# Kernel optimization log

Measured on AMD Instinct MI355X. Metric: run time of the kernel, lower is better.

The kernel has to match this reference:

```python
import jax, jax.numpy as jnp
import numpy as np

B, T, S, D, H, FF = 4, 1024, 1024, 1024, 16, 4096
DH = D // H
NEG = -1e9
EPS = 1e-5


def setup_inputs() -> dict:
    key = jax.random.key(0)
    ks = jax.random.split(key, 20)
    p = 0.02  # param init scale
    inp = {
        "x": jax.random.normal(ks[0], (B, T, D), jnp.float32),
        "encoder_output": jax.random.normal(ks[1], (B, S, D), jnp.float32),
        "src_mask": jnp.ones((B, 1, 1, S), jnp.bool_),
        "tgt_mask": jnp.tril(jnp.ones((1, 1, T, T), jnp.bool_)),  # causal
        # self-attention params
        "d_Wq": jax.random.normal(ks[2], (D, D)) * p, "d_bq": jnp.zeros((D,)),
        "d_Wk": jax.random.normal(ks[3], (D, D)) * p, "d_bk": jnp.zeros((D,)),
        "d_Wv": jax.random.normal(ks[4], (D, D)) * p, "d_bv": jnp.zeros((D,)),
        "d_Wo": jax.random.normal(ks[5], (D, D)) * p, "d_bo": jnp.zeros((D,)),
        # cross-attention params
        "e_Wq": jax.random.normal(ks[6], (D, D)) * p, "e_bq": jnp.zeros((D,)),
        "e_Wk": jax.random.normal(ks[7], (D, D)) * p, "e_bk": jnp.zeros((D,)),
        "e_Wv": jax.random.normal(ks[8], (D, D)) * p, "e_bv": jnp.zeros((D,)),
        "e_Wo": jax.random.normal(ks[9], (D, D)) * p, "e_bo": jnp.zeros((D,)),
        # FFN params
        "ff_W1": jax.random.normal(ks[10], (D, FF)) * p, "ff_b1": jnp.zeros((FF,)),
        "ff_W2": jax.random.normal(ks[11], (FF, D)) * p, "ff_b2": jnp.zeros((D,)),
        # layernorm params
        "ln1_g": jnp.ones((D,)), "ln1_b": jnp.zeros((D,)),
        "ln2_g": jnp.ones((D,)), "ln2_b": jnp.zeros((D,)),
        "ln3_g": jnp.ones((D,)), "ln3_b": jnp.zeros((D,)),
    }
    return inp


def _mha(xq, xkv, Wq, bq, Wk, bk, Wv, bv, Wo, bo, mask):
    b, tq = xq.shape[0], xq.shape[1]
    q = (xq @ Wq + bq).reshape(b, tq, H, DH).transpose(0, 2, 1, 3)
    k = (xkv @ Wk + bk).reshape(b, -1, H, DH).transpose(0, 2, 1, 3)
    v = (xkv @ Wv + bv).reshape(b, -1, H, DH).transpose(0, 2, 1, 3)
    scores = jnp.einsum("bhqd,bhkd->bhqk", q, k) / np.float32(np.sqrt(DH))
    scores = jnp.where(mask, scores, NEG)
    attn = jax.nn.softmax(scores, axis=-1)
    out = jnp.einsum("bhqk,bhkd->bhqd", attn, v)
    out = out.transpose(0, 2, 1, 3).reshape(b, tq, D)
    return out @ Wo + bo


def _ln(x, g, b):
    m = jnp.mean(x, axis=-1, keepdims=True)
    v = jnp.var(x, axis=-1, keepdims=True)
    return (x - m) / jnp.sqrt(v + EPS) * g + b


def reference(x, encoder_output, src_mask, tgt_mask,
              d_Wq, d_bq, d_Wk, d_bk, d_Wv, d_bv, d_Wo, d_bo,
              e_Wq, e_bq, e_Wk, e_bk, e_Wv, e_bv, e_Wo, e_bo,
              ff_W1, ff_b1, ff_W2, ff_b2,
              ln1_g, ln1_b, ln2_g, ln2_b, ln3_g, ln3_b):
    # masked self-attention + residual + LN (dropout is identity in eval)
    d = _mha(x, x, d_Wq, d_bq, d_Wk, d_bk, d_Wv, d_bv, d_Wo, d_bo, tgt_mask)
    d = _ln(d + x, ln1_g, ln1_b)
    # cross-attention over encoder output + residual + LN
    f = _mha(d, encoder_output, e_Wq, e_bq, e_Wk, e_bk, e_Wv, e_bv, e_Wo, e_bo, src_mask)
    f = _ln(f + d, ln2_g, ln2_b)
    # FFN + residual + LN
    g = jax.nn.relu(f @ ff_W1 + ff_b1) @ ff_W2 + ff_b2
    g = _ln(g + f, ln3_g, ln3_b)
    return g
```

## Files before the change

### kernel.cpp

```cpp
#include <hip/hip_runtime.h>

static constexpr int Bc = 4, Tc = 1024, Sc = 1024, Dc = 1024, Hc = 16, DHc = 64, FFc = 4096;

typedef __attribute__((ext_vector_type(8))) short short8;
typedef __attribute__((ext_vector_type(4))) short short4v;
typedef __attribute__((ext_vector_type(4))) float f32x4;

struct P8 { unsigned short* o[8]; };

__device__ __forceinline__ unsigned short f2bf(float f) {
    unsigned int u = __float_as_uint(f);
    unsigned int r = u + 0x7fffu + ((u >> 16) & 1u);
    return (unsigned short)(r >> 16);
}
__device__ __forceinline__ float bf2f(unsigned short u) {
    return __uint_as_float(((unsigned int)u) << 16);
}
__device__ __forceinline__ float fexp2(float x) {
    float r; asm("v_exp_f32 %0, %1" : "=v"(r) : "v"(x)); return r;
}
__device__ __forceinline__ unsigned int cvtpk(float a, float b) {
    unsigned int r;
    asm("v_cvt_pk_bf16_f32 %0, %1, %2" : "=v"(r) : "v"(a), "v"(b));
    return r;
}

__device__ __forceinline__ void gload_lds16(const void* g, void* l) {
    __builtin_amdgcn_global_load_lds((const __attribute__((address_space(1))) void*)g,
                                     (__attribute__((address_space(3))) void*)l, 16, 0, 0);
}

__global__ __launch_bounds__(256) void cast2_f32_bf16(const float* __restrict__ inA,
                                                      const float* __restrict__ inB,
                                                      unsigned short* __restrict__ outA,
                                                      unsigned short* __restrict__ outB, int n8) {
    int i = blockIdx.x * 256 + threadIdx.x;
    if (i >= n8) return;
    const float* in = blockIdx.y ? inB : inA;
    unsigned short* out = blockIdx.y ? outB : outA;
    const float4* p = (const float4*)in + (size_t)i * 2;
    float4 a = p[0], b = p[1];
    short8 o;
    o[0] = f2bf(a.x); o[1] = f2bf(a.y); o[2] = f2bf(a.z); o[3] = f2bf(a.w);
    o[4] = f2bf(b.x); o[5] = f2bf(b.y); o[6] = f2bf(b.z); o[7] = f2bf(b.w);
    *(short8*)(out + (size_t)i * 8) = o;
}

struct TJ { const float* s; unsigned short* d; int ss, ds; float scl; };
struct TJ16 { TJ j[16]; };
__global__ __launch_bounds__(256) void transpose_cast16(TJ16 p) {
    __shared__ float t[64][65];
    const TJ jb = p.j[blockIdx.z];
    const int c0 = blockIdx.x * 64, r0 = blockIdx.y * 64;
    const int tid = threadIdx.x;
    const int rr = tid >> 2, cc = (tid & 3) * 16;
    const float* src = jb.s + (size_t)(r0 + rr) * jb.ss + c0 + cc;
#pragma unroll
    for (int i = 0; i < 4; i++) {
        float4 v = *(const float4*)(src + i * 4);
        t[rr][cc + i * 4 + 0] = v.x;
        t[rr][cc + i * 4 + 1] = v.y;
        t[rr][cc + i * 4 + 2] = v.z;
        t[rr][cc + i * 4 + 3] = v.w;
    }
    __syncthreads();
#pragma unroll
    for (int half = 0; half < 2; half++) {
        const int id = half * 256 + tid;
        const int a = id >> 3, b0 = id & 7;
        short8 o;
#pragma unroll
        for (int e = 0; e < 8; e++) o[e] = f2bf(t[b0 * 8 + e][a] * jb.scl);
        *(short8*)(jb.d + (size_t)(c0 + a) * jb.ds + r0 + b0 * 8) = o;
    }
}

__global__ void prep_bias(const float* dbq, const float* dbk, const float* dbv,
                          const float* ebk, const float* ebv, const float* ebq,
                          float* __restrict__ bqkv, float* __restrict__ bekv,
                          float* __restrict__ ebq_s, float SC) {
    int i = blockIdx.x * 256 + threadIdx.x;
    int seg = i >> 10, j = i & 1023;
    switch (seg) {
        case 0: bqkv[j] = dbq[j] * SC; break;
        case 1: bqkv[1024 + j] = dbk[j]; break;
        case 2: bqkv[2048 + j] = dbv[j]; break;
        case 3: bekv[j] = ebk[j]; break;
        case 4: bekv[1024 + j] = ebv[j]; break;
        default: ebq_s[j] = ebq[j] * SC; break;
    }
}

__global__ __launch_bounds__(256) void combineKV(unsigned short* __restrict__ kv,
                                                 const unsigned short* __restrict__ p1,
                                                 unsigned short* __restrict__ Vt) {
    __shared__ unsigned short t[64 * 64];
    const int bx = blockIdx.x;
    const int tid = threadIdx.x;
    if (bx < 2048) {
        const int cid = bx * 256 + tid;
        const int row = cid >> 7, col8 = (cid & 127) * 8;
        const size_t a = (size_t)row * 2048 + col8;
        short8 x = *(short8*)(kv + a);
        short8 y = *(const short8*)(p1 + a);
        short8 o;
#pragma unroll
        for (int j = 0; j < 8; j++)
            o[j] = f2bf(bf2f((unsigned short)x[j]) + bf2f((unsigned short)y[j]));
        *(short8*)(kv + a) = o;
        return;
    }
    const int vb = bx - 2048;
    const int bh = vb & 63, b = bh >> 4, h = bh & 15;
    const int s0 = (vb >> 6) * 64;
    const int r = tid >> 2, ch = tid & 3;
    const size_t off = (size_t)(b * 1024 + s0 + r) * 2048 + 1024 + h * 64 + ch * 16;
    short8 x0 = *(const short8*)(kv + off);
    short8 x1 = *(const short8*)(kv + off + 8);
    short8 y0 = *(const short8*)(p1 + off);
    short8 y1 = *(const short8*)(p1 + off + 8);
    short8 v0, v1;
#pragma unroll
    for (int j = 0; j < 8; j++) {
        v0[j] = f2bf(bf2f((unsigned short)x0[j]) + bf2f((unsigned short)y0[j]));
        v1[j] = f2bf(bf2f((unsigned short)x1[j]) + bf2f((unsigned short)y1[j]));
    }
    int pw_ = (ch ^ r ^ (r >> 4)) & 3;
    *(short8*)(t + r * 64 + pw_ * 16) = v0;
    *(short8*)(t + r * 64 + pw_ * 16 + 8) = v1;
    __syncthreads();
    const int dh = tid >> 2, sc = (tid & 3) * 16;
    short8 o0, o1;
#pragma unroll
    for (int j = 0; j < 8; j++) {
        int c0 = sc + j, c1 = sc + 8 + j;
        o0[j] = t[c0 * 64 + (((dh >> 4) ^ c0 ^ (c0 >> 4)) & 3) * 16 + (dh & 15)];
        o1[j] = t[c1 * 64 + (((dh >> 4) ^ c1 ^ (c1 >> 4)) & 3) * 16 + (dh & 15)];
    }
    unsigned short* dst = Vt + ((size_t)bh * 64 + dh) * 1024 + s0 + sc;
    *(short8*)dst = o0;
    *(short8*)(dst + 8) = o1;
}

struct BlkMap { int m, n, z; };
__device__ __forceinline__ BlkMap remap_block() {
    const int gx = gridDim.x, gy = gridDim.y;
    const int nxy = gx * gy;
    const int nwg = nxy * gridDim.z;
    const int flat = (blockIdx.z * gy + blockIdx.y) * gx + blockIdx.x;
    const int id = (flat & 7) * (nwg >> 3) + (flat >> 3);
    const int pz = id / nxy;
    const int rz = id - pz * nxy;
    const int gwsh = (gx & 7) ? 2 : 3;
    const int gw = 1 << gwsh;
    const int gsz = gw * gy;
    const int grp = rz / gsz;
    const int rem = rz - grp * gsz;
    BlkMap r;
    r.m = rem >> gwsh;
    r.n = (grp << gwsh) + (rem & (gw - 1));
    r.z = pz;
    return r;
}

template <int EPI>
__global__ __launch_bounds__(512, 2) void gemm256(const unsigned short* __restrict__ A,
                                                  const unsigned short* __restrict__ Bt,
                                                  const float* __restrict__ bias,
                                                  unsigned short* __restrict__ outB,
                                                  int N, int lda, int ldb, int nk, P8 po) {
    __shared__ unsigned short SM[2][2][2][8192];
    const int tid = threadIdx.x;
    const int lane = tid & 63, wid = tid >> 6;
    const int l4 = lane & 15, g = lane >> 4;
    const int wr = wid >> 2, wc = wid & 3;
    BlkMap bm = remap_block();
    const int m0 = bm.m * 256, n0 = bm.n * 256, z = bm.z;
    A += (size_t)z * (nk * 64);
    Bt += (size_t)z * (nk * 64);
    const int sw = l4 & 7;

    const int fl0 = tid, fl1 = 512 + tid;
    const int lr0 = fl0 >> 3, ch0 = (fl0 & 7) ^ (lr0 & 7);
    const int lr1 = fl1 >> 3, ch1 = (fl1 & 7) ^ (lr1 & 7);
    const size_t A64 = (size_t)64 * lda;
    const unsigned short* pA0 = A + (size_t)(m0 + (lr0 >> 6) * 128 + (lr0 & 63)) * lda + ch0 * 8;
    const unsigned short* pA1 = A + (size_t)(m0 + (lr1 >> 6) * 128 + (lr1 & 63)) * lda + ch1 * 8;
    const unsigned short* pB0 = Bt + (size_t)(n0 + (ch0 >> 2) * 128 + lr0) * ldb + (ch0 & 3) * 8;
    const unsigned short* pB1 = Bt + (size_t)(n0 + (ch1 >> 2) * 128 + lr1) * ldb + (ch1 & 3) * 8;

    auto stA = [&](int d, int mh, int kofs) {
        char* base = (char*)&SM[0][d][mh][0];
        gload_lds16(pA0 + (size_t)mh * A64 + kofs, base + fl0 * 16);
        gload_lds16(pA1 + (size_t)mh * A64 + kofs, base + fl1 * 16);
    };
    auto stB = [&](int d, int ks, int kofs) {
        char* base = (char*)&SM[1][d][ks][0];
        gload_lds16(pB0 + ks * 32 + kofs, base + fl0 * 16);
        gload_lds16(pB1 + ks * 32 + kofs, base + fl1 * 16);
    };

    f32x4 acc[8][4] = {};
    short8 aF[4], aH[4], b0[4], b1[4];

    auto ldA = [&](int d, int mh, short8* d0, short8* d1) {
#pragma unroll
        for (int m = 0; m < 4; m++) {
            const char* rp = (const char*)&SM[0][d][mh][0] + (wr * 64 + m * 16 + l4) * 128;
            d0[m] = *(const short8*)(rp + ((g ^ sw) * 16));
            d1[m] = *(const short8*)(rp + (((4 + g) ^ sw) * 16));
        }
    };
    auto ldB = [&](int d, int ks, short8* dst) {
#pragma unroll
        for (int n = 0; n < 4; n++) {
            const char* rp = (const char*)&SM[1][d][ks][0] + ((wc & 1) * 64 + n * 16 + l4) * 128;
            dst[n] = *(const short8*)(rp + ((((wc >> 1) * 4 + g) ^ sw) * 16));
        }
    };

#define MFMA16(aa, bb, base)                                                                  \
    _Pragma("unroll") for (int m_ = 0; m_ < 4; m_++)                                          \
        _Pragma("unroll") for (int n_ = 0; n_ < 4; n_++)                                      \
            acc[(base) + m_][n_] = __builtin_amdgcn_mfma_f32_16x16x32_bf16(                   \
                (aa)[m_], (bb)[n_], acc[(base) + m_][n_], 0, 0, 0);

    stB(0, 0, 0); stA(0, 0, 0); stB(0, 1, 0); stA(0, 1, 0);
    stB(1, 0, 64); stA(1, 0, 64); stB(1, 1, 64);
    asm volatile("s_waitcnt vmcnt(6)" ::: "memory");
    __builtin_amdgcn_s_barrier();

    const int nIter = nk >> 1;
    for (int it = 0; it < nIter; ++it) {
        const int t = 2 * it, u = t + 1;
        const int ku = u * 64;
        const int kv = ((t + 2 < nk) ? t + 2 : t) * 64;
        const int kw = ((u + 2 < nk) ? u + 2 : u) * 64;
        ldB(0, 0, b0); ldA(0, 0, aF, aH);
        stA(1, 1, ku);
        asm volatile("s_waitcnt lgkmcnt(8)" ::: "memory");
        __builtin_amdgcn_s_barrier();
        asm volatile("s_waitcnt lgkmcnt(0)" ::: "memory");
        __builtin_amdgcn_s_setprio(1); MFMA16(aF, b0, 0); __builtin_amdgcn_s_setprio(0);
        __builtin_amdgcn_s_barrier();
        ldB(0, 1, b1);
        stB(0, 0, kv);
        __builtin_amdgcn_s_barrier();
        asm volatile("s_waitcnt lgkmcnt(0)" ::: "memory");
        __builtin_amdgcn_s_setprio(1); MFMA16(aH, b1, 0); __builtin_amdgcn_s_setprio(0);
        __builtin_amdgcn_s_barrier();
        ldA(0, 1, aF, aH);
        stA(0, 0, kv);
        __builtin_amdgcn_s_barrier();
        asm volatile("s_waitcnt lgkmcnt(0)" ::: "memory");
        __builtin_amdgcn_s_setprio(1); MFMA16(aH, b1, 4); __builtin_amdgcn_s_setprio(0);
        __builtin_amdgcn_s_barrier();
        stB(0, 1, kv);
        __builtin_amdgcn_s_barrier();
        __builtin_amdgcn_s_setprio(1); MFMA16(aF, b0, 4); __builtin_amdgcn_s_setprio(0);
        asm volatile("s_waitcnt vmcnt(6)" ::: "memory");
        __builtin_amdgcn_s_barrier();
        ldB(1, 0, b0); ldA(1, 0, aF, aH);
        stA(0, 1, kv);
        asm volatile("s_waitcnt lgkmcnt(8)" ::: "memory");
        __builtin_amdgcn_s_barrier();
        asm volatile("s_waitcnt lgkmcnt(0)" ::: "memory");
        __builtin_amdgcn_s_setprio(1); MFMA16(aF, b0, 0); __builtin_amdgcn_s_setprio(0);
        __builtin_amdgcn_s_barrier();
        ldB(1, 1, b1);
        stB(1, 0, kw);
        __builtin_amdgcn_s_barrier();
        asm volatile("s_waitcnt lgkmcnt(0)" ::: "memory");
        __builtin_amdgcn_s_setprio(1); MFMA16(aH, b1, 0); __builtin_amdgcn_s_setprio(0);
        __builtin_amdgcn_s_barrier();
        ldA(1, 1, aF, aH);
        stA(1, 0, kw);
        __builtin_amdgcn_s_barrier();
        asm volatile("s_waitcnt lgkmcnt(0)" ::: "memory");
        __builtin_amdgcn_s_setprio(1); MFMA16(aH, b1, 4); __builtin_amdgcn_s_setprio(0);
        __builtin_amdgcn_s_barrier();
        stB(1, 1, kw);
        __builtin_amdgcn_s_barrier();
        __builtin_amdgcn_s_setprio(1); MFMA16(aF, b0, 4); __builtin_amdgcn_s_setprio(0);
        asm volatile("s_waitcnt vmcnt(6)" ::: "memory");
        __builtin_amdgcn_s_barrier();
    }
    asm volatile("s_waitcnt vmcnt(0)" ::: "memory");
    __syncthreads();

    unsigned short* eb = (unsigned short*)SM;
    unsigned short* oB = (EPI == 3) ? po.o[z] : outB;
    const int colL = wc * 64 + l4;
#pragma unroll
    for (int h = 0; h < 2; ++h) {
        if (wr == h) {
#pragma unroll
            for (int mm = 0; mm < 8; mm++) {
                const int base_r = (mm < 4 ? mm * 16 : 64 + (mm - 4) * 16) + g * 4;
#pragma unroll
                for (int n = 0; n < 4; n++) {
                    float bv = (EPI == 3 && z != 0) ? 0.f : bias[n0 + colL + n * 16];
#pragma unroll
                    for (int r = 0; r < 4; r++) {
                        float v = acc[mm][n][r] + bv;
                        if (EPI == 2) v = fmaxf(v, 0.f);
                        eb[(base_r + r) * 260 + colL + n * 16] = f2bf(v);
                    }
                }
            }
        }
        __syncthreads();
        const int gr0 = m0 + h * 128;
        if (EPI == 4 && n0 >= 2048) {
            const int b_ = gr0 >> 10, sb = gr0 & 1023;
#pragma unroll
            for (int j = 0; j < 4; j++) {
                const int id = j * 512 + tid;
                const int col = id & 255, rseg = id >> 8;
                const int rel = n0 - 2048 + col;
                const int hh = rel >> 6, dh = rel & 63;
                short8 v0, v1;
#pragma unroll
                for (int e = 0; e < 8; e++) {
                    v0[e] = eb[(rseg * 16 + e) * 260 + col];
                    v1[e] = eb[(rseg * 16 + 8 + e) * 260 + col];
                }
                unsigned short* dp = po.o[0] +
                    ((size_t)(b_ * 16 + hh) * 64 + dh) * 1024 + sb + rseg * 16;
                *(short8*)dp = v0;
                *(short8*)(dp + 8) = v1;
            }
        } else {
#pragma unroll
            for (int j = 0; j < 8; j++) {
                const int f = j * 8192 + tid * 16;
                const int row = f >> 9;
                const int colb = f & 511;
                short8 v = *(const short8*)((const char*)eb + row * 520 + colb);
                *(short8*)(oB + (size_t)(gr0 + row) * N + n0 + (colb >> 1)) = v;
            }
        }
        if (h == 0) __syncthreads();
    }
#undef MFMA16
}

template <int EPI>
__global__ __launch_bounds__(256) void gemm64_db(const unsigned short* __restrict__ A,
                                                 const unsigned short* __restrict__ Bt,
                                                 const float* __restrict__ bias,
                                                 float* __restrict__ outF,
                                                 unsigned short* __restrict__ outB,
                                                 int M, int N, int Kloop, int lda, int ldb) {
    __shared__ unsigned short As[3][64 * 32];
    __shared__ unsigned short Bs[3][128 * 32];
    const int tid = threadIdx.x;
    const int w = tid >> 6, lane = tid & 63, l4 = lane & 15, g = lane >> 4;
    BlkMap bm = remap_block();
    const int m0 = bm.m * 64, n0 = bm.n * 128;
    f32x4 acc[4][2] = {};
    const int r0 = tid >> 2;
    const int kk = ((tid & 3) ^ ((tid >> 3) & 3)) * 8;
    const int sk = (l4 >> 1) & 3;
    const unsigned short* Ar0 = A + (size_t)(m0 + r0) * lda + kk;
    const unsigned short* Br0 = Bt + (size_t)(n0 + r0) * ldb + kk;
    const unsigned short* Br1 = Bt + (size_t)(n0 + 64 + r0) * ldb + kk;
    auto stage = [&](int sb, int k0) {
        gload_lds16(Ar0 + k0, (char*)As[sb] + tid * 16);
        gload_lds16(Br0 + k0, (char*)Bs[sb] + tid * 16);
        gload_lds16(Br1 + k0, (char*)Bs[sb] + 4096 + tid * 16);
    };
    const int nk = Kloop >> 5;
    stage(0, 0);
    stage(1, 32);
    asm volatile("s_waitcnt vmcnt(3)" ::: "memory");
    __builtin_amdgcn_s_barrier();
    asm volatile("" ::: "memory");
    int buf = 0;
    for (int t = 0; t < nk; ++t) {
        if (t + 2 < nk) {
            int b2 = buf + 2; if (b2 >= 3) b2 -= 3;
            stage(b2, (t + 2) * 32);
        }
        short8 a[4], b[2];
#pragma unroll
        for (int m = 0; m < 4; m++)
            a[m] = *(const short8*)(As[buf] + (m * 16 + l4) * 32 + (g ^ sk) * 8);
#pragma unroll
        for (int n = 0; n < 2; n++)
            b[n] = *(const short8*)(Bs[buf] + (w * 32 + n * 16 + l4) * 32 + (g ^ sk) * 8);
#pragma unroll
        for (int m = 0; m < 4; m++)
#pragma unroll
            for (int n = 0; n < 2; n++)
                acc[m][n] = __builtin_amdgcn_mfma_f32_16x16x32_bf16(a[m], b[n], acc[m][n], 0, 0, 0);
        if (t + 1 < nk) {
            if (t + 2 < nk) asm volatile("s_waitcnt vmcnt(3)" ::: "memory");
            else            asm volatile("s_waitcnt vmcnt(0)" ::: "memory");
            __builtin_amdgcn_s_barrier();
            asm volatile("" ::: "memory");
        }
        buf = (buf + 1 == 3) ? 0 : buf + 1;
    }
    const int rowB = m0 + g * 4;
    const int colB = n0 + w * 32 + l4;
#pragma unroll
    for (int n = 0; n < 2; n++) {
        float bv = bias[colB + n * 16];
#pragma unroll
        for (int m = 0; m < 4; m++) {
#pragma unroll
            for (int r = 0; r < 4; r++) {
                float v = acc[m][n][r] + bv;
                if (EPI == 2) v = fmaxf(v, 0.f);
                size_t idx = (size_t)(rowB + m * 16 + r) * N + colB + n * 16;
                if (EPI == 1) outF[idx] = v;
                else outB[idx] = f2bf(v);
            }
        }
    }
}

template <int CAUSAL>
__global__ __launch_bounds__(512) void attn6_kernel(const unsigned short* __restrict__ Q, int ldq,
                                                    const unsigned short* __restrict__ Kg, int ldk,
                                                    const unsigned short* __restrict__ Vt,
                                                    unsigned short* __restrict__ O) {
    __shared__ unsigned short Kl[2 * 64 * 64];
    __shared__ unsigned short Vl[2 * 64 * 64];
    __shared__ unsigned short Pl[8][16 * 72];
    const int bh = blockIdx.x;
    const int qb = CAUSAL ? (gridDim.y - 1 - blockIdx.y) : blockIdx.y;
    const int b = bh >> 4, h = bh & 15;
    const int tid = threadIdx.x, w = tid >> 6, lane = tid & 63;
    const int l4 = lane & 15, g = lane >> 4;
    const int q0 = qb * 128 + w * 16;
    const unsigned short* Qp = Q + (size_t)(b * Tc + q0 + l4) * ldq + h * DHc + g * 8;
    short8 qf0 = *(const short8*)Qp;
    short8 qf1 = *(const short8*)(Qp + 32);
    const unsigned short* Kbase = Kg + (size_t)(b * 1024) * ldk + h * DHc;
    const unsigned short* Vbase = Vt + (size_t)bh * DHc * 1024;
    f32x4 o[4] = {};
    float mrun = -1e30f, lrun = 0.f;
    const int nT = CAUSAL ? 2 * qb + 2 : 16;
    unsigned short* pw = &Pl[w][l4 * 72];
    const int qi = q0 + l4;

    short8 ones;
#pragma unroll
    for (int j = 0; j < 8; j++) ones[j] = (short)0x3F80;

    const int sr = tid >> 3;
    const int sc_ = (tid & 7) ^ (sr & 7);

    auto stage = [&](int s0, int buf) {
        char* kd = (char*)Kl + buf * 8192;
        char* vd = (char*)Vl + buf * 8192;
        gload_lds16(Kbase + (size_t)(s0 + sr) * ldk + sc_ * 8, kd + tid * 16);
        gload_lds16(Vbase + (size_t)sr * 1024 + s0 + sc_ * 8, vd + tid * 16);
    };

    stage(0, 0);
    __syncthreads();
    int buf = 0;
    const int sw = l4 & 7;

    for (int t = 0; t < nT; ++t) {
        const int s0 = t * 64;
        if (t + 1 < nT) stage(s0 + 64, buf ^ 1);
        if (!CAUSAL || s0 <= q0 + 15) {
            const unsigned short* Kb_ = Kl + buf * 4096;
            const unsigned short* Vb_ = Vl + buf * 4096;
            f32x4 st[4];
            f32x4 z = {0.f, 0.f, 0.f, 0.f};
            __builtin_amdgcn_s_setprio(1);
#pragma unroll
            for (int c = 0; c < 4; c++) {
                const unsigned short* kr = Kb_ + (c * 16 + l4) * 64;
                short8 ka0 = *(const short8*)(kr + ((g ^ sw) * 8));
                short8 ka1 = *(const short8*)(kr + (((g + 4) ^ sw) * 8));
                st[c] = __builtin_amdgcn_mfma_f32_16x16x32_bf16(ka0, qf0, z, 0, 0, 0);
                st[c] = __builtin_amdgcn_mfma_f32_16x16x32_bf16(ka1, qf1, st[c], 0, 0, 0);
            }
            __builtin_amdgcn_s_setprio(0);
            float p[16];
            const bool domask = CAUSAL && (s0 + 63 > q0);
#pragma unroll
            for (int c = 0; c < 4; c++)
#pragma unroll
                for (int r = 0; r < 4; r++) {
                    float v = st[c][r];
                    if (domask && (s0 + c * 16 + g * 4 + r) > qi) v = -1e9f;
                    p[c * 4 + r] = v;
                }
            float m1 = fmaxf(fmaxf(p[0], p[1]), p[2]);
            float m2 = fmaxf(fmaxf(p[3], p[4]), p[5]);
            float m3 = fmaxf(fmaxf(p[6], p[7]), p[8]);
            float m4 = fmaxf(fmaxf(p[9], p[10]), p[11]);
            float m5 = fmaxf(fmaxf(p[12], p[13]), p[14]);
            float tmax = fmaxf(fmaxf(fmaxf(m1, m2), fmaxf(m3, m4)), fmaxf(m5, p[15]));
            tmax = fmaxf(tmax, __shfl_xor(tmax, 16));
            tmax = fmaxf(tmax, __shfl_xor(tmax, 32));
            if (!__all(tmax <= mrun + 11.5f)) {
                float mnew = fmaxf(mrun, tmax);
                float al = fexp2(mrun - mnew);
                lrun *= al;
#pragma unroll
                for (int d = 0; d < 4; d++) o[d] *= al;
                mrun = mnew;
            }
#pragma unroll
            for (int i = 0; i < 16; i++) p[i] = fexp2(p[i] - mrun);
#pragma unroll
            for (int c = 0; c < 4; c++) {
                uint2 u;
                u.x = cvtpk(p[c * 4 + 0], p[c * 4 + 1]);
                u.y = cvtpk(p[c * 4 + 2], p[c * 4 + 3]);
                *(uint2*)(pw + c * 16 + g * 4) = u;
            }
            short8 pb_lo = *(const short8*)(pw + g * 8);
            short8 pb_hi = *(const short8*)(pw + 32 + g * 8);
            __builtin_amdgcn_s_setprio(1);
            f32x4 s4 = __builtin_amdgcn_mfma_f32_16x16x32_bf16(ones, pb_lo, z, 0, 0, 0);
            s4 = __builtin_amdgcn_mfma_f32_16x16x32_bf16(ones, pb_hi, s4, 0, 0, 0);
#pragma unroll
            for (int d = 0; d < 4; d++) {
                const unsigned short* vr = Vb_ + (d * 16 + l4) * 64;
                short8 va0 = *(const short8*)(vr + ((g ^ sw) * 8));
                short8 va1 = *(const short8*)(vr + (((g + 4) ^ sw) * 8));
                o[d] = __builtin_amdgcn_mfma_f32_16x16x32_bf16(va0, pb_lo, o[d], 0, 0, 0);
                o[d] = __builtin_amdgcn_mfma_f32_16x16x32_bf16(va1, pb_hi, o[d], 0, 0, 0);
            }
            __builtin_amdgcn_s_setprio(0);
            lrun += s4[0];
        }
        __syncthreads();
        buf ^= 1;
    }
    float inv = 1.f / lrun;
    unsigned short* Ob = O + (size_t)(b * Tc + q0 + l4) * Dc + h * DHc;
#pragma unroll
    for (int d = 0; d < 4; d++) {
#pragma unroll
        for (int r = 0; r < 4; r++) Ob[d * 16 + g * 4 + r] = f2bf(o[d][r] * inv);
    }
}

__global__ __launch_bounds__(256) void ln_bf(const unsigned short* __restrict__ a,
                                             const unsigned short* __restrict__ res,
                                             const float* __restrict__ gam,
                                             const float* __restrict__ bet,
                                             unsigned short* __restrict__ outB,
                                             float* __restrict__ outF) {
    int row = blockIdx.x, t = threadIdx.x;
    size_t base = (size_t)row * Dc + t * 4;
    short4v av = *(const short4v*)(a + base);
    short4v rv = *(const short4v*)(res + base);
    float x0 = bf2f((unsigned short)av[0]) + bf2f((unsigned short)rv[0]);
    float x1 = bf2f((unsigned short)av[1]) + bf2f((unsigned short)rv[1]);
    float x2 = bf2f((unsigned short)av[2]) + bf2f((unsigned short)rv[2]);
    float x3 = bf2f((unsigned short)av[3]) + bf2f((unsigned short)rv[3]);
    float s = x0 + x1 + x2 + x3;
    float ss = x0 * x0 + x1 * x1 + x2 * x2 + x3 * x3;
    for (int o = 1; o < 64; o <<= 1) { s += __shfl_xor(s, o); ss += __shfl_xor(ss, o); }
    __shared__ float S1[4], S2[4];
    int w = t >> 6;
    if ((t & 63) == 0) { S1[w] = s; S2[w] = ss; }
    __syncthreads();
    s = S1[0] + S1[1] + S1[2] + S1[3];
    ss = S2[0] + S2[1] + S2[2] + S2[3];
    float mean = s * (1.f / Dc);
    float var = ss * (1.f / Dc) - mean * mean;
    float rstd = rsqrtf(var + 1e-5f);
    int c = t * 4;
    float4 g4 = *(const float4*)(gam + c);
    float4 b4 = *(const float4*)(bet + c);
    float y0 = (x0 - mean) * rstd * g4.x + b4.x;
    float y1 = (x1 - mean) * rstd * g4.y + b4.y;
    float y2 = (x2 - mean) * rstd * g4.z + b4.z;
    float y3 = (x3 - mean) * rstd * g4.w + b4.w;
    if (outB) {
        short4v ob;
        ob[0] = f2bf(y0); ob[1] = f2bf(y1); ob[2] = f2bf(y2); ob[3] = f2bf(y3);
        *(short4v*)(outB + base) = ob;
    }
    if (outF) { float4 ov = {y0, y1, y2, y3}; *(float4*)(outF + base) = ov; }
}

__global__ __launch_bounds__(256) void ln_4b(const unsigned short* __restrict__ p,
                                             const unsigned short* __restrict__ res,
                                             const float* __restrict__ gam,
                                             const float* __restrict__ bet,
                                             float* __restrict__ outF) {
    const size_t PS = (size_t)4096 * 1024;
    int row = blockIdx.x, t = threadIdx.x;
    size_t base = (size_t)row * Dc + t * 4;
    float x0, x1, x2, x3;
    {
        short4v rv = *(const short4v*)(res + base);
        x0 = bf2f((unsigned short)rv[0]); x1 = bf2f((unsigned short)rv[1]);
        x2 = bf2f((unsigned short)rv[2]); x3 = bf2f((unsigned short)rv[3]);
    }
#pragma unroll
    for (int j = 0; j < 4; j++) {
        short4v v = *(const short4v*)(p + j * PS + base);
        x0 += bf2f((unsigned short)v[0]); x1 += bf2f((unsigned short)v[1]);
        x2 += bf2f((unsigned short)v[2]); x3 += bf2f((unsigned short)v[3]);
    }
    float s = x0 + x1 + x2 + x3;
    float ss = x0 * x0 + x1 * x1 + x2 * x2 + x3 * x3;
    for (int o = 1; o < 64; o <<= 1) { s += __shfl_xor(s, o); ss += __shfl_xor(ss, o); }
    __shared__ float S1[4], S2[4];
    int w = t >> 6;
    if ((t & 63) == 0) { S1[w] = s; S2[w] = ss; }
    __syncthreads();
    s = S1[0] + S1[1] + S1[2] + S1[3];
    ss = S2[0] + S2[1] + S2[2] + S2[3];
    float mean = s * (1.f / Dc);
    float var = ss * (1.f / Dc) - mean * mean;
    float rstd = rsqrtf(var + 1e-5f);
    int c = t * 4;
    float4 g4 = *(const float4*)(gam + c);
    float4 b4 = *(const float4*)(bet + c);
    float4 ov;
    ov.x = (x0 - mean) * rstd * g4.x + b4.x;
    ov.y = (x1 - mean) * rstd * g4.y + b4.y;
    ov.z = (x2 - mean) * rstd * g4.z + b4.z;
    ov.w = (x3 - mean) * rstd * g4.w + b4.w;
    *(float4*)(outF + base) = ov;
}

extern "C" void kernel_launch(void* const* d_in, const int* in_sizes, int n_in,
                              void* d_out, int out_size, void* d_ws, size_t ws_size,
                              hipStream_t stream) {
    const float* x   = (const float*)d_in[0];
    const float* enc = (const float*)d_in[1];
    const float* dWq = (const float*)d_in[4];  const float* dbq = (const float*)d_in[5];
    const float* dWk = (const float*)d_in[6];  const float* dbk = (const float*)d_in[7];
    const float* dWv = (const float*)d_in[8];  const float* dbv = (const float*)d_in[9];
    const float* dWo = (const float*)d_in[10]; const float* dbo = (const float*)d_in[11];
    const float* eWq = (const float*)d_in[12]; const float* ebq = (const float*)d_in[13];
    const float* eWk = (const float*)d_in[14]; const float* ebk = (const float*)d_in[15];
    const float* eWv = (const float*)d_in[16]; const float* ebv = (const float*)d_in[17];
    const float* eWo = (const float*)d_in[18]; const float* ebo = (const float*)d_in[19];
    const float* fW1 = (const float*)d_in[20]; const float* fb1 = (const float*)d_in[21];
    const float* fW2 = (const float*)d_in[22]; const float* fb2 = (const float*)d_in[23];
    const float* g1 = (const float*)d_in[24];  const float* be1 = (const float*)d_in[25];
    const float* g2 = (const float*)d_in[26];  const float* be2 = (const float*)d_in[27];
    const float* g3 = (const float*)d_in[28];  const float* be3 = (const float*)d_in[29];

    const float SC = 0.125f * 1.44269504f;

    char* ws = (char*)d_ws;
    size_t off = 0;
    auto alloc = [&](size_t bytes) -> void* {
        void* p = ws + off;
        off += (bytes + 255) & ~(size_t)255;
        return p;
    };
    const size_t A = (size_t)4096 * 1024;
    const size_t MB1 = (size_t)1024 * 1024;
    char* R1 = (char*)alloc(32 * 1024 * 1024);
    unsigned short* qkv = (unsigned short*)R1;
    unsigned short* kvx = (unsigned short*)R1;
    unsigned short* qx  = (unsigned short*)(R1 + 16 * 1024 * 1024);
    unsigned short* h1  = (unsigned short*)R1;
    unsigned short* xb   = (unsigned short*)alloc(A * 2);
    unsigned short* encb = (unsigned short*)alloc(A * 2);
    unsigned short* wqkv = (unsigned short*)alloc(3 * MB1 * 2);
    unsigned short* wekv = (unsigned short*)alloc(2 * MB1 * 2);
    unsigned short* weq  = (unsigned short*)alloc(MB1 * 2);
    unsigned short* wdo  = (unsigned short*)alloc(MB1 * 2);
    unsigned short* weo  = (unsigned short*)alloc(MB1 * 2);
    unsigned short* wf1  = (unsigned short*)alloc(4 * MB1 * 2);
    unsigned short* wf2  = (unsigned short*)alloc(4 * MB1 * 2);
    float* bqkv = (float*)alloc(3072 * 4);
    float* bekv = (float*)alloc(2048 * 4);
    float* ebq_s = (float*)alloc(1024 * 4);
    unsigned short* VtB = (unsigned short*)alloc(A * 2);
    unsigned short* ab  = (unsigned short*)alloc(A * 2);
    unsigned short* tmpB = (unsigned short*)alloc(A * 2);
    unsigned short* dB = (unsigned short*)alloc(A * 2);
    unsigned short* fB = (unsigned short*)alloc(A * 2);
    unsigned short* pfb = VtB;
    (void)ws_size; (void)in_sizes; (void)n_in; (void)out_size;

    cast2_f32_bf16<<<dim3(2048, 2), 256, 0, stream>>>(x, enc, xb, encb, (int)(A / 8));

    TJ16 tj;
    tj.j[0] = {dWq, wqkv,           1024, 1024, SC};
    tj.j[1] = {dWk, wqkv + MB1,     1024, 1024, 1.f};
    tj.j[2] = {dWv, wqkv + 2 * MB1, 1024, 1024, 1.f};
    tj.j[3] = {eWk, wekv,           1024, 1024, 1.f};
    tj.j[4] = {eWv, wekv + MB1,     1024, 1024, 1.f};
    tj.j[5] = {eWq, weq,            1024, 1024, SC};
    tj.j[6] = {dWo, wdo,            1024, 1024, 1.f};
    tj.j[7] = {eWo, weo,            1024, 1024, 1.f};
    for (int jj = 0; jj < 4; jj++) {
        tj.j[8 + jj]  = {fW1 + 1024 * jj, wf1 + (size_t)1024 * jj * 1024, 4096, 1024, 1.f};
        tj.j[12 + jj] = {fW2 + (size_t)1024 * jj * 1024, wf2 + 1024 * jj, 1024, 4096, 1.f};
    }
    transpose_cast16<<<dim3(16, 16, 16), 256, 0, stream>>>(tj);
    prep_bias<<<24, 256, 0, stream>>>(dbq, dbk, dbv, ebk, ebv, ebq, bqkv, bekv, ebq_s, SC);

    P8 z8{};

    {
        P8 pq{};
        pq.o[0] = VtB;
        gemm256<4><<<dim3(12, 16), 512, 0, stream>>>(xb, wqkv, bqkv, qkv, 3072, 1024, 1024, 16, pq);
    }
    attn6_kernel<1><<<dim3(64, 8), 512, 0, stream>>>(qkv, 3072, qkv + 1024, 3072, VtB, ab);
    gemm64_db<0><<<dim3(8, 64), 256, 0, stream>>>(ab, wdo, dbo, nullptr, tmpB, 4096, 1024, 1024, 1024, 1024);
    ln_bf<<<4096, 256, 0, stream>>>(tmpB, xb, g1, be1, dB, nullptr);

    {
        P8 pe{};
        pe.o[0] = kvx;
        pe.o[1] = VtB;
        gemm256<3><<<dim3(8, 16, 2), 512, 0, stream>>>(encb, wekv, bekv, nullptr, 2048, 1024, 1024, 8, pe);
        combineKV<<<3072, 256, 0, stream>>>(kvx, VtB, tmpB);
    }
    gemm64_db<0><<<dim3(8, 64), 256, 0, stream>>>(dB, weq, ebq_s, nullptr, qx, 4096, 1024, 1024, 1024, 1024);
    attn6_kernel<0><<<dim3(64, 8), 512, 0, stream>>>(qx, 1024, kvx, 2048, tmpB, ab);
    gemm64_db<0><<<dim3(8, 64), 256, 0, stream>>>(ab, weo, ebo, nullptr, tmpB, 4096, 1024, 1024, 1024, 1024);
    ln_bf<<<4096, 256, 0, stream>>>(tmpB, dB, g2, be2, fB, nullptr);

    gemm256<2><<<dim3(16, 16), 512, 0, stream>>>(fB, wf1, fb1, h1, 4096, 1024, 1024, 16, z8);
    {
        P8 pf{};
        pf.o[0] = pfb;
        pf.o[1] = pfb + A;
        pf.o[2] = pfb + 2 * A;
        pf.o[3] = pfb + 3 * A;
        gemm256<3><<<dim3(4, 16, 4), 512, 0, stream>>>(h1, wf2, fb2, nullptr, 1024, 4096, 4096, 16, pf);
    }
    ln_4b<<<4096, 256, 0, stream>>>(pfb, fB, g3, be3, (float*)d_out);
}
```

Baseline: 320.1 us.

## Merge self-attn QKV and cross-attn KV GEMMs into one grouped launch

New measurement: 313.8 us (median of 3 runs). 2.0% less time.

```diff
diff --git a/kernel.cpp b/kernel.cpp
--- a/kernel.cpp
+++ b/kernel.cpp
@@ -89,57 +89,6 @@
         case 4: bekv[1024 + j] = ebv[j]; break;
         default: ebq_s[j] = ebq[j] * SC; break;
     }
-}
-
-__global__ __launch_bounds__(256) void combineKV(unsigned short* __restrict__ kv,
-                                                 const unsigned short* __restrict__ p1,
-                                                 unsigned short* __restrict__ Vt) {
-    __shared__ unsigned short t[64 * 64];
-    const int bx = blockIdx.x;
-    const int tid = threadIdx.x;
-    if (bx < 2048) {
-        const int cid = bx * 256 + tid;
-        const int row = cid >> 7, col8 = (cid & 127) * 8;
-        const size_t a = (size_t)row * 2048 + col8;
-        short8 x = *(short8*)(kv + a);
-        short8 y = *(const short8*)(p1 + a);
-        short8 o;
-#pragma unroll
-        for (int j = 0; j < 8; j++)
-            o[j] = f2bf(bf2f((unsigned short)x[j]) + bf2f((unsigned short)y[j]));
-        *(short8*)(kv + a) = o;
-        return;
-    }
-    const int vb = bx - 2048;
-    const int bh = vb & 63, b = bh >> 4, h = bh & 15;
-    const int s0 = (vb >> 6) * 64;
-    const int r = tid >> 2, ch = tid & 3;
-    const size_t off = (size_t)(b * 1024 + s0 + r) * 2048 + 1024 + h * 64 + ch * 16;
-    short8 x0 = *(const short8*)(kv + off);
-    short8 x1 = *(const short8*)(kv + off + 8);
-    short8 y0 = *(const short8*)(p1 + off);
-    short8 y1 = *(const short8*)(p1 + off + 8);
-    short8 v0, v1;
-#pragma unroll
-    for (int j = 0; j < 8; j++) {
-        v0[j] = f2bf(bf2f((unsigned short)x0[j]) + bf2f((unsigned short)y0[j]));
-        v1[j] = f2bf(bf2f((unsigned short)x1[j]) + bf2f((unsigned short)y1[j]));
-    }
-    int pw_ = (ch ^ r ^ (r >> 4)) & 3;
-    *(short8*)(t + r * 64 + pw_ * 16) = v0;
-    *(short8*)(t + r * 64 + pw_ * 16 + 8) = v1;
-    __syncthreads();
-    const int dh = tid >> 2, sc = (tid & 3) * 16;
-    short8 o0, o1;
-#pragma unroll
-    for (int j = 0; j < 8; j++) {
-        int c0 = sc + j, c1 = sc + 8 + j;
-        o0[j] = t[c0 * 64 + (((dh >> 4) ^ c0 ^ (c0 >> 4)) & 3) * 16 + (dh & 15)];
-        o1[j] = t[c1 * 64 + (((dh >> 4) ^ c1 ^ (c1 >> 4)) & 3) * 16 + (dh & 15)];
-    }
-    unsigned short* dst = Vt + ((size_t)bh * 64 + dh) * 1024 + s0 + sc;
-    *(short8*)dst = o0;
-    *(short8*)(dst + 8) = o1;
 }
 
 struct BlkMap { int m, n, z; };
@@ -163,6 +112,75 @@
     return r;
 }
 
+#define G256_BODY()                                                                            \
+    stB(0, 0, 0); stA(0, 0, 0); stB(0, 1, 0); stA(0, 1, 0);                                    \
+    stB(1, 0, 64); stA(1, 0, 64); stB(1, 1, 64);                                               \
+    asm volatile("s_waitcnt vmcnt(6)" ::: "memory");                                           \
+    __builtin_amdgcn_s_barrier();                                                              \
+    const int nIter = nk >> 1;                                                                 \
+    for (int it = 0; it < nIter; ++it) {                                                       \
+        const int t_ = 2 * it, u_ = t_ + 1;                                                    \
+        const int ku = u_ * 64;                                                                \
+        const int kv = ((t_ + 2 < nk) ? t_ + 2 : t_) * 64;                                     \
+        const int kw = ((u_ + 2 < nk) ? u_ + 2 : u_) * 64;                                     \
+        ldB(0, 0, b0); ldA(0, 0, aF, aH);                                                      \
+        stA(1, 1, ku);                                                                         \
+        asm volatile("s_waitcnt lgkmcnt(8)" ::: "memory");                                     \
+        __builtin_amdgcn_s_barrier();                                                          \
+        asm volatile("s_waitcnt lgkmcnt(0)" ::: "memory");                                     \
+        __builtin_amdgcn_s_setprio(1); MFMA16(aF, b0, 0); __builtin_amdgcn_s_setprio(0);       \
+        __builtin_amdgcn_s_barrier();                                                          \
+        ldB(0, 1, b1);                                                                         \
+        stB(0, 0, kv);                                                                         \
+        __builtin_amdgcn_s_barrier();                                                          \
+        asm volatile("s_waitcnt lgkmcnt(0)" ::: "memory");                                     \
+        __builtin_amdgcn_s_setprio(1); MFMA16(aH, b1, 0); __builtin_amdgcn_s_setprio(0);       \
+        __builtin_amdgcn_s_barrier();                                                          \
+        ldA(0, 1, aF, aH);                                                                     \
+        stA(0, 0, kv);                                                                         \
+        __builtin_amdgcn_s_barrier();                                                          \
+        asm volatile("s_waitcnt lgkmcnt(0)" ::: "memory");                                     \
+        __builtin_amdgcn_s_setprio(1); MFMA16(aH, b1, 4); __builtin_amdgcn_s_setprio(0);       \
+        __builtin_amdgcn_s_barrier();                                                          \
+        stB(0, 1, kv);                                                                         \
+        __builtin_amdgcn_s_barrier();                                                          \
+        __builtin_amdgcn_s_setprio(1); MFMA16(aF, b0, 4); __builtin_amdgcn_s_setprio(0);       \
+        asm volatile("s_waitcnt vmcnt(6)" ::: "memory");                                       \
+        __builtin_amdgcn_s_barrier();                                                          \
+        ldB(1, 0, b0); ldA(1, 0, aF, aH);                                                      \
+        stA(0, 1, kv);                                                                         \
+        asm volatile("s_waitcnt lgkmcnt(8)" ::: "memory");                                     \
+        __builtin_amdgcn_s_barrier();                                                          \
+        asm volatile("s_waitcnt lgkmcnt(0)" ::: "memory");                                     \
+        __builtin_amdgcn_s_setprio(1); MFMA16(aF, b0, 0); __builtin_amdgcn_s_setprio(0);       \
+        __builtin_amdgcn_s_barrier();                                                          \
+        ldB(1, 1, b1);                                                                         \
+        stB(1, 0, kw);                                                                         \
+        __builtin_amdgcn_s_barrier();                                                          \
+        asm volatile("s_waitcnt lgkmcnt(0)" ::: "memory");                                     \
+        __builtin_amdgcn_s_setprio(1); MFMA16(aH, b1, 0); __builtin_amdgcn_s_setprio(0);       \
+        __builtin_amdgcn_s_barrier();                                                          \
+        ldA(1, 1, aF, aH);                                                                     \
+        stA(1, 0, kw);                                                                         \
+        __builtin_amdgcn_s_barrier();                                                          \
+        asm volatile("s_waitcnt lgkmcnt(0)" ::: "memory");                                     \
+        __builtin_amdgcn_s_setprio(1); MFMA16(aH, b1, 4); __builtin_amdgcn_s_setprio(0);       \
+        __builtin_amdgcn_s_barrier();                                                          \
+        stB(1, 1, kw);                                                                         \
+        __builtin_amdgcn_s_barrier();                                                          \
+        __builtin_amdgcn_s_setprio(1); MFMA16(aF, b0, 4); __builtin_amdgcn_s_setprio(0);       \
+        asm volatile("s_waitcnt vmcnt(6)" ::: "memory");                                       \
+        __builtin_amdgcn_s_barrier();                                                          \
+    }                                                                                          \
+    asm volatile("s_waitcnt vmcnt(0)" ::: "memory");                                           \
+    __syncthreads();
+
+#define MFMA16(aa, bb, base)                                                                   \
+    _Pragma("unroll") for (int m_ = 0; m_ < 4; m_++)                                           \
+        _Pragma("unroll") for (int n_ = 0; n_ < 4; n_++)                                       \
+            acc[(base) + m_][n_] = __builtin_amdgcn_mfma_f32_16x16x32_bf16(                    \
+                (aa)[m_], (bb)[n_], acc[(base) + m_][n_], 0, 0, 0);
+
 template <int EPI>
 __global__ __launch_bounds__(512, 2) void gemm256(const unsigned short* __restrict__ A,
                                                   const unsigned short* __restrict__ Bt,
@@ -219,74 +237,7 @@
         }
     };
 
-#define MFMA16(aa, bb, base)                                                                  \
-    _Pragma("unroll") for (int m_ = 0; m_ < 4; m_++)                                          \
-        _Pragma("unroll") for (int n_ = 0; n_ < 4; n_++)                                      \
-            acc[(base) + m_][n_] = __builtin_amdgcn_mfma_f32_16x16x32_bf16(                   \
-                (aa)[m_], (bb)[n_], acc[(base) + m_][n_], 0, 0, 0);
-
-    stB(0, 0, 0); stA(0, 0, 0); stB(0, 1, 0); stA(0, 1, 0);
-    stB(1, 0, 64); stA(1, 0, 64); stB(1, 1, 64);
-    asm volatile("s_waitcnt vmcnt(6)" ::: "memory");
-    __builtin_amdgcn_s_barrier();
-
-    const int nIter = nk >> 1;
-    for (int it = 0; it < nIter; ++it) {
-        const int t = 2 * it, u = t + 1;
-        const int ku = u * 64;
-        const int kv = ((t + 2 < nk) ? t + 2 : t) * 64;
-        const int kw = ((u + 2 < nk) ? u + 2 : u) * 64;
-        ldB(0, 0, b0); ldA(0, 0, aF, aH);
-        stA(1, 1, ku);
-        asm volatile("s_waitcnt lgkmcnt(8)" ::: "memory");
-        __builtin_amdgcn_s_barrier();
-        asm volatile("s_waitcnt lgkmcnt(0)" ::: "memory");
-        __builtin_amdgcn_s_setprio(1); MFMA16(aF, b0, 0); __builtin_amdgcn_s_setprio(0);
-        __builtin_amdgcn_s_barrier();
-        ldB(0, 1, b1);
-        stB(0, 0, kv);
-        __builtin_amdgcn_s_barrier();
-        asm volatile("s_waitcnt lgkmcnt(0)" ::: "memory");
-        __builtin_amdgcn_s_setprio(1); MFMA16(aH, b1, 0); __builtin_amdgcn_s_setprio(0);
-        __builtin_amdgcn_s_barrier();
-        ldA(0, 1, aF, aH);
-        stA(0, 0, kv);
-        __builtin_amdgcn_s_barrier();
-        asm volatile("s_waitcnt lgkmcnt(0)" ::: "memory");
-        __builtin_amdgcn_s_setprio(1); MFMA16(aH, b1, 4); __builtin_amdgcn_s_setprio(0);
-        __builtin_amdgcn_s_barrier();
-        stB(0, 1, kv);
-        __builtin_amdgcn_s_barrier();
-        __builtin_amdgcn_s_setprio(1); MFMA16(aF, b0, 4); __builtin_amdgcn_s_setprio(0);
-        asm volatile("s_waitcnt vmcnt(6)" ::: "memory");
-        __builtin_amdgcn_s_barrier();
-        ldB(1, 0, b0); ldA(1, 0, aF, aH);
-        stA(0, 1, kv);
-        asm volatile("s_waitcnt lgkmcnt(8)" ::: "memory");
-        __builtin_amdgcn_s_barrier();
-        asm volatile("s_waitcnt lgkmcnt(0)" ::: "memory");
-        __builtin_amdgcn_s_setprio(1); MFMA16(aF, b0, 0); __builtin_amdgcn_s_setprio(0);
-        __builtin_amdgcn_s_barrier();
-        ldB(1, 1, b1);
-        stB(1, 0, kw);
-        __builtin_amdgcn_s_barrier();
-        asm volatile("s_waitcnt lgkmcnt(0)" ::: "memory");
-        __builtin_amdgcn_s_setprio(1); MFMA16(aH, b1, 0); __builtin_amdgcn_s_setprio(0);
-        __builtin_amdgcn_s_barrier();
-        ldA(1, 1, aF, aH);
-        stA(1, 0, kw);
-        __builtin_amdgcn_s_barrier();
-        asm volatile("s_waitcnt lgkmcnt(0)" ::: "memory");
-        __builtin_amdgcn_s_setprio(1); MFMA16(aH, b1, 4); __builtin_amdgcn_s_setprio(0);
-        __builtin_amdgcn_s_barrier();
-        stB(1, 1, kw);
-        __builtin_amdgcn_s_barrier();
-        __builtin_amdgcn_s_setprio(1); MFMA16(aF, b0, 4); __builtin_amdgcn_s_setprio(0);
-        asm volatile("s_waitcnt vmcnt(6)" ::: "memory");
-        __builtin_amdgcn_s_barrier();
-    }
-    asm volatile("s_waitcnt vmcnt(0)" ::: "memory");
-    __syncthreads();
+    G256_BODY()
 
     unsigned short* eb = (unsigned short*)SM;
     unsigned short* oB = (EPI == 3) ? po.o[z] : outB;
@@ -311,13 +262,118 @@
         }
         __syncthreads();
         const int gr0 = m0 + h * 128;
-        if (EPI == 4 && n0 >= 2048) {
+#pragma unroll
+        for (int j = 0; j < 8; j++) {
+            const int f = j * 8192 + tid * 16;
+            const int row = f >> 9;
+            const int colb = f & 511;
+            short8 v = *(const short8*)((const char*)eb + row * 520 + colb);
+            *(short8*)(oB + (size_t)(gr0 + row) * N + n0 + (colb >> 1)) = v;
+        }
+        if (h == 0) __syncthreads();
+    }
+}
+
+struct GJob {
+    const unsigned short *A, *Bt;
+    const float* bias;
+    unsigned short *out, *vt;
+    int N, lda, ldb, nk, vthresh, nwg, gx;
+};
+struct GJ2 { GJob j[2]; };
+__global__ __launch_bounds__(512, 2) void gemm256j(GJ2 p) {
+    __shared__ unsigned short SM[2][2][2][8192];
+    const int tid = threadIdx.x;
+    const int lane = tid & 63, wid = tid >> 6;
+    const int l4 = lane & 15, g = lane >> 4;
+    const int wr = wid >> 2, wc = wid & 3;
+
+    int f = blockIdx.x;
+    const int ji = (f < p.j[0].nwg) ? 0 : 1;
+    if (ji) f -= p.j[0].nwg;
+    const GJob jb = p.j[ji];
+    const int id = (f & 7) * (jb.nwg >> 3) + (f >> 3);
+    const int gwsh = (jb.gx & 7) ? 2 : 3;
+    const int gw = 1 << gwsh;
+    const int gy = jb.nwg / jb.gx;
+    const int gsz = gw * gy;
+    const int grp = id / gsz;
+    const int rem = id - grp * gsz;
+    const int m0 = (rem >> gwsh) * 256;
+    const int n0 = ((grp << gwsh) + (rem & (gw - 1))) * 256;
+
+    const unsigned short* A = jb.A;
+    const unsigned short* Bt = jb.Bt;
+    const int lda = jb.lda, ldb = jb.ldb, nk = jb.nk;
+    const int sw = l4 & 7;
+
+    const int fl0 = tid, fl1 = 512 + tid;
+    const int lr0 = fl0 >> 3, ch0 = (fl0 & 7) ^ (lr0 & 7);
+    const int lr1 = fl1 >> 3, ch1 = (fl1 & 7) ^ (lr1 & 7);
+    const size_t A64 = (size_t)64 * lda;
+    const unsigned short* pA0 = A + (size_t)(m0 + (lr0 >> 6) * 128 + (lr0 & 63)) * lda + ch0 * 8;
+    const unsigned short* pA1 = A + (size_t)(m0 + (lr1 >> 6) * 128 + (lr1 & 63)) * lda + ch1 * 8;
+    const unsigned short* pB0 = Bt + (size_t)(n0 + (ch0 >> 2) * 128 + lr0) * ldb + (ch0 & 3) * 8;
+    const unsigned short* pB1 = Bt + (size_t)(n0 + (ch1 >> 2) * 128 + lr1) * ldb + (ch1 & 3) * 8;
+
+    auto stA = [&](int d, int mh, int kofs) {
+        char* base = (char*)&SM[0][d][mh][0];
+        gload_lds16(pA0 + (size_t)mh * A64 + kofs, base + fl0 * 16);
+        gload_lds16(pA1 + (size_t)mh * A64 + kofs, base + fl1 * 16);
+    };
+    auto stB = [&](int d, int ks, int kofs) {
+        char* base = (char*)&SM[1][d][ks][0];
+        gload_lds16(pB0 + ks * 32 + kofs, base + fl0 * 16);
+        gload_lds16(pB1 + ks * 32 + kofs, base + fl1 * 16);
+    };
+
+    f32x4 acc[8][4] = {};
+    short8 aF[4], aH[4], b0[4], b1[4];
+
+    auto ldA = [&](int d, int mh, short8* d0, short8* d1) {
+#pragma unroll
+        for (int m = 0; m < 4; m++) {
+            const char* rp = (const char*)&SM[0][d][mh][0] + (wr * 64 + m * 16 + l4) * 128;
+            d0[m] = *(const short8*)(rp + ((g ^ sw) * 16));
+            d1[m] = *(const short8*)(rp + (((4 + g) ^ sw) * 16));
+        }
+    };
+    auto ldB = [&](int d, int ks, short8* dst) {
+#pragma unroll
+        for (int n = 0; n < 4; n++) {
+            const char* rp = (const char*)&SM[1][d][ks][0] + ((wc & 1) * 64 + n * 16 + l4) * 128;
+            dst[n] = *(const short8*)(rp + ((((wc >> 1) * 4 + g) ^ sw) * 16));
+        }
+    };
+
+    G256_BODY()
+
+    unsigned short* eb = (unsigned short*)SM;
+    const int colL = wc * 64 + l4;
+#pragma unroll
+    for (int h = 0; h < 2; ++h) {
+        if (wr == h) {
+#pragma unroll
+            for (int mm = 0; mm < 8; mm++) {
+                const int base_r = (mm < 4 ? mm * 16 : 64 + (mm - 4) * 16) + g * 4;
+#pragma unroll
+                for (int n = 0; n < 4; n++) {
+                    float bv = jb.bias[n0 + colL + n * 16];
+#pragma unroll
+                    for (int r = 0; r < 4; r++)
+                        eb[(base_r + r) * 260 + colL + n * 16] = f2bf(acc[mm][n][r] + bv);
+                }
+            }
+        }
+        __syncthreads();
+        const int gr0 = m0 + h * 128;
+        if (n0 >= jb.vthresh) {
             const int b_ = gr0 >> 10, sb = gr0 & 1023;
 #pragma unroll
             for (int j = 0; j < 4; j++) {
-                const int id = j * 512 + tid;
-                const int col = id & 255, rseg = id >> 8;
-                const int rel = n0 - 2048 + col;
+                const int id2 = j * 512 + tid;
+                const int col = id2 & 255, rseg = id2 >> 8;
+                const int rel = n0 - jb.vthresh + col;
                 const int hh = rel >> 6, dh = rel & 63;
                 short8 v0, v1;
 #pragma unroll
@@ -325,7 +381,7 @@
                     v0[e] = eb[(rseg * 16 + e) * 260 + col];
                     v1[e] = eb[(rseg * 16 + 8 + e) * 260 + col];
                 }
-                unsigned short* dp = po.o[0] +
+                unsigned short* dp = jb.vt +
                     ((size_t)(b_ * 16 + hh) * 64 + dh) * 1024 + sb + rseg * 16;
                 *(short8*)dp = v0;
                 *(short8*)(dp + 8) = v1;
@@ -333,16 +389,15 @@
         } else {
 #pragma unroll
             for (int j = 0; j < 8; j++) {
-                const int f = j * 8192 + tid * 16;
-                const int row = f >> 9;
-                const int colb = f & 511;
+                const int ff = j * 8192 + tid * 16;
+                const int row = ff >> 9;
+                const int colb = ff & 511;
                 short8 v = *(const short8*)((const char*)eb + row * 520 + colb);
-                *(short8*)(oB + (size_t)(gr0 + row) * N + n0 + (colb >> 1)) = v;
+                *(short8*)(jb.out + (size_t)(gr0 + row) * jb.N + n0 + (colb >> 1)) = v;
             }
         }
         if (h == 0) __syncthreads();
     }
-#undef MFMA16
 }
 
 template <int EPI>
@@ -662,7 +717,6 @@
     const size_t MB1 = (size_t)1024 * 1024;
     char* R1 = (char*)alloc(32 * 1024 * 1024);
     unsigned short* qkv = (unsigned short*)R1;
-    unsigned short* kvx = (unsigned short*)R1;
     unsigned short* qx  = (unsigned short*)(R1 + 16 * 1024 * 1024);
     unsigned short* h1  = (unsigned short*)R1;
     unsigned short* xb   = (unsigned short*)alloc(A * 2);
@@ -682,6 +736,8 @@
     unsigned short* tmpB = (unsigned short*)alloc(A * 2);
     unsigned short* dB = (unsigned short*)alloc(A * 2);
     unsigned short* fB = (unsigned short*)alloc(A * 2);
+    unsigned short* kb  = (unsigned short*)alloc(A * 2);
+    unsigned short* vtc = (unsigned short*)alloc(A * 2);
     unsigned short* pfb = VtB;
     (void)ws_size; (void)in_sizes; (void)n_in; (void)out_size;
 
@@ -706,23 +762,18 @@
     P8 z8{};
 
     {
-        P8 pq{};
-        pq.o[0] = VtB;
-        gemm256<4><<<dim3(12, 16), 512, 0, stream>>>(xb, wqkv, bqkv, qkv, 3072, 1024, 1024, 16, pq);
-    }
+        GJ2 gj;
+        gj.j[0] = {xb, wqkv, bqkv, qkv, VtB, 3072, 1024, 1024, 16, 2048, 192, 12};
+        gj.j[1] = {encb, wekv, bekv, kb, vtc, 1024, 1024, 1024, 16, 1024, 128, 8};
+        gemm256j<<<dim3(320), 512, 0, stream>>>(gj);
+    }
+
     attn6_kernel<1><<<dim3(64, 8), 512, 0, stream>>>(qkv, 3072, qkv + 1024, 3072, VtB, ab);
     gemm64_db<0><<<dim3(8, 64), 256, 0, stream>>>(ab, wdo, dbo, nullptr, tmpB, 4096, 1024, 1024, 1024, 1024);
     ln_bf<<<4096, 256, 0, stream>>>(tmpB, xb, g1, be1, dB, nullptr);
 
-    {
-        P8 pe{};
-        pe.o[0] = kvx;
-        pe.o[1] = VtB;
-        gemm256<3><<<dim3(8, 16, 2), 512, 0, stream>>>(encb, wekv, bekv, nullptr, 2048, 1024, 1024, 8, pe);
-        combineKV<<<3072, 256, 0, stream>>>(kvx, VtB, tmpB);
-    }
     gemm64_db<0><<<dim3(8, 64), 256, 0, stream>>>(dB, weq, ebq_s, nullptr, qx, 4096, 1024, 1024, 1024, 1024);
-    attn6_kernel<0><<<dim3(64, 8), 512, 0, stream>>>(qx, 1024, kvx, 2048, tmpB, ab);
+    attn6_kernel<0><<<dim3(64, 8), 512, 0, stream>>>(qx, 1024, kb, 1024, vtc, ab);
     gemm64_db<0><<<dim3(8, 64), 256, 0, stream>>>(ab, weo, ebo, nullptr, tmpB, 4096, 1024, 1024, 1024, 1024);
     ln_bf<<<4096, 256, 0, stream>>>(tmpB, dB, g2, be2, fB, nullptr);
 
```
